# Performance work log

Hardware: AMD Instinct MI355X
Metric: run time of the kernel (lower is better)

The kernel has to match this reference:

```python
import jax, jax.numpy as jnp
import numpy as np

B, D_TCF, T, GAF_DIM, DK, HIDDEN, N_CLASSES = 128, 512, 1024, 256, 32, 64, 4
EPS = 1e-5

def _glorot(key, shape):
    fan_out, fan_in = shape
    lim = float(np.sqrt(6.0 / (fan_in + fan_out)))
    return jax.random.uniform(key, shape, jnp.float32, -lim, lim)

def setup_inputs() -> dict:
    key = jax.random.key(0)
    ks = jax.random.split(key, 8)
    return {
        "tcf_feat": jax.random.normal(ks[0], (B, D_TCF, T), jnp.float32),
        "gaf_emb": jax.random.normal(ks[1], (B, GAF_DIM), jnp.float32),
        "Wq": _glorot(ks[2], (DK, D_TCF)),        # q_proj.weight [out,in]
        "Wkv": _glorot(ks[3], (DK, GAF_DIM)),     # kv_proj.weight
        "Wout": _glorot(ks[4], (D_TCF, DK)),      # out_proj.weight
        "ln1_g": jnp.ones((D_TCF,), jnp.float32),
        "ln1_b": jnp.zeros((D_TCF,), jnp.float32),
        "W1": _glorot(ks[5], (HIDDEN, D_TCF)),
        "b1": jnp.zeros((HIDDEN,), jnp.float32),
        "ln2_g": jnp.ones((HIDDEN,), jnp.float32),
        "ln2_b": jnp.zeros((HIDDEN,), jnp.float32),
        "W2": _glorot(ks[6], (N_CLASSES, HIDDEN)),
        "b2": jnp.zeros((N_CLASSES,), jnp.float32),
    }

def _layernorm(x, g, b):
    mu = jnp.mean(x, axis=-1, keepdims=True)
    var = jnp.mean(jnp.square(x - mu), axis=-1, keepdims=True)
    return (x - mu) * jax.lax.rsqrt(var + EPS) * g + b

def reference(tcf_feat, gaf_emb, Wq, Wkv, Wout, ln1_g, ln1_b, W1, b1, ln2_g, ln2_b, W2, b2):
    scale = DK ** (-0.5)
    x = jnp.swapaxes(tcf_feat, 1, 2)                      # [B,T,d_tcf]
    Q = jnp.einsum('btd,kd->btk', x, Wq)                  # [B,T,dk]
    KV = gaf_emb @ Wkv.T                                  # [B,dk] (single key/value)
    scores = jnp.einsum('btk,bk->bt', Q, KV) * scale      # [B,T]
    w = jax.nn.softmax(scores, axis=1)                    # softmax over T (dim=1)
    attn_out = w[:, :, None] * KV[:, None, :]             # [B,T,dk]
    y = _layernorm(x + jnp.einsum('btk,dk->btd', attn_out, Wout), ln1_g, ln1_b)
    pooled = jnp.mean(y, axis=1)                          # [B,d_tcf]
    h = jax.nn.elu(_layernorm(pooled @ W1.T + b1, ln2_g, ln2_b))
    return h @ W2.T + b2                                  # [B,n_classes]
```

## Files before the change

kernel.cpp:

```cpp
#include <hip/hip_runtime.h>

#define BN 128
#define DTCF 512
#define TT 1024
#define GAF 256
#define DKK 32
#define HID 64
#define NCLS 4
#define LNEPS 1e-5f

__global__ __launch_bounds__(256) void k_prep(
    const float* __restrict__ gaf, const float* __restrict__ Wq,
    const float* __restrict__ Wkv, const float* __restrict__ Wout,
    float* __restrict__ u, float* __restrict__ qv,
    float* __restrict__ muu, float* __restrict__ varu)
{
    int b = blockIdx.x, tid = threadIdx.x;
    __shared__ float gaf_s[GAF];
    __shared__ float kv_s[DKK];
    __shared__ float red[16];

    gaf_s[tid & (GAF - 1)] = gaf[b * GAF + (tid & (GAF - 1))];
    __syncthreads();

    if (tid < DKK) {
        float acc = 0.f;
        for (int g = 0; g < GAF; ++g) acc += gaf_s[g] * Wkv[tid * GAF + g];
        kv_s[tid] = acc;
    }
    __syncthreads();

    float su = 0.f, suu = 0.f;
    for (int d = tid; d < DTCF; d += 256) {
        float uu = 0.f, qq = 0.f;
        #pragma unroll
        for (int k = 0; k < DKK; ++k) {
            float kv = kv_s[k];
            uu += kv * Wout[d * DKK + k];
            qq += kv * Wq[k * DTCF + d];
        }
        u[b * DTCF + d] = uu;
        qv[b * DTCF + d] = qq;
        su += uu; suu += uu * uu;
    }
    int lane = tid & 63, wv = tid >> 6;
    for (int off = 32; off > 0; off >>= 1) {
        su  += __shfl_down(su, off);
        suu += __shfl_down(suu, off);
    }
    if (lane == 0) { red[wv] = su; red[8 + wv] = suu; }
    __syncthreads();
    if (tid == 0) {
        float s  = red[0] + red[1] + red[2] + red[3];
        float ss = red[8] + red[9] + red[10] + red[11];
        float m = s * (1.f / DTCF);
        muu[b]  = m;
        varu[b] = ss * (1.f / DTCF) - m * m;
    }
}

__global__ __launch_bounds__(256) void k_passA(
    const float* __restrict__ tcf, const float* __restrict__ u,
    const float* __restrict__ qv, const float* __restrict__ muu,
    float* __restrict__ mx_o, float* __restrict__ varx_o,
    float* __restrict__ cov_o, float* __restrict__ score_o)
{
    int b = blockIdx.x, tc = blockIdx.y, tid = threadIdx.x;
    int t = tc * 256 + tid;
    __shared__ float u_s[DTCF], qv_s[DTCF];
    for (int i = tid; i < DTCF; i += 256) {
        u_s[i]  = u[b * DTCF + i];
        qv_s[i] = qv[b * DTCF + i];
    }
    __syncthreads();

    const float* base = tcf + (size_t)b * DTCF * TT + t;
    float sx = 0.f, sxx = 0.f, sxu = 0.f, sxq = 0.f;
    #pragma unroll 8
    for (int d = 0; d < DTCF; ++d) {
        float v = base[(size_t)d * TT];
        sx  += v;
        sxx += v * v;
        sxu += v * u_s[d];
        sxq += v * qv_s[d];
    }
    float mx = sx * (1.f / DTCF);
    size_t o = (size_t)b * TT + t;
    mx_o[o]    = mx;
    varx_o[o]  = sxx * (1.f / DTCF) - mx * mx;
    cov_o[o]   = sxu * (1.f / DTCF) - mx * muu[b];
    score_o[o] = sxq * 0.17677669529663687f;
}

__global__ __launch_bounds__(256) void k_soft(
    const float* __restrict__ score, const float* __restrict__ varx,
    const float* __restrict__ cov, const float* __restrict__ mx,
    const float* __restrict__ varu,
    float* __restrict__ r_o, float* __restrict__ S2, float* __restrict__ S3)
{
    int b = blockIdx.x, tid = threadIdx.x;
    int lane = tid & 63, wv = tid >> 6;
    __shared__ float red[16];
    const float* sc = score + (size_t)b * TT;

    float s0 = sc[tid], s1 = sc[tid + 256], s2v = sc[tid + 512], s3v = sc[tid + 768];
    float m = fmaxf(fmaxf(s0, s1), fmaxf(s2v, s3v));
    for (int off = 32; off > 0; off >>= 1) m = fmaxf(m, __shfl_xor(m, off));
    if (lane == 0) red[wv] = m;
    __syncthreads();
    m = fmaxf(fmaxf(red[0], red[1]), fmaxf(red[2], red[3]));

    float e0 = __expf(s0 - m), e1 = __expf(s1 - m);
    float e2 = __expf(s2v - m), e3 = __expf(s3v - m);
    float sum = e0 + e1 + e2 + e3;
    for (int off = 32; off > 0; off >>= 1) sum += __shfl_xor(sum, off);
    __syncthreads();
    if (lane == 0) red[4 + wv] = sum;
    __syncthreads();
    sum = red[4] + red[5] + red[6] + red[7];
    float inv = 1.f / sum;
    float vu = varu[b];

    float e[4] = {e0, e1, e2, e3};
    float s2a = 0.f, s3a = 0.f;
    #pragma unroll
    for (int i = 0; i < 4; ++i) {
        size_t o = (size_t)b * TT + tid + i * 256;
        float w = e[i] * inv;
        float vr = varx[o] + 2.f * w * cov[o] + w * w * vu;
        float rr = rsqrtf(vr + LNEPS);
        r_o[o] = rr;
        s2a += rr * w;
        s3a += rr * mx[o];
    }
    for (int off = 32; off > 0; off >>= 1) {
        s2a += __shfl_xor(s2a, off);
        s3a += __shfl_xor(s3a, off);
    }
    __syncthreads();
    if (lane == 0) { red[wv] = s2a; red[8 + wv] = s3a; }
    __syncthreads();
    if (tid == 0) {
        S2[b] = (red[0] + red[1] + red[2] + red[3]) * (1.f / TT);
        S3[b] = (red[8] + red[9] + red[10] + red[11]) * (1.f / TT);
    }
}

__global__ __launch_bounds__(256) void k_passB(
    const float* __restrict__ tcf, const float* __restrict__ r,
    const float* __restrict__ u, const float* __restrict__ muu,
    const float* __restrict__ S2, const float* __restrict__ S3,
    const float* __restrict__ g1, const float* __restrict__ be1,
    float* __restrict__ pooled)
{
    int b = blockIdx.x, dblk = blockIdx.y;
    int tid = threadIdx.x, wv = tid >> 6, lane = tid & 63;
    int d = dblk * 4 + wv;

    const float* row = tcf + ((size_t)b * DTCF + d) * TT + lane * 16;
    const float* rb  = r + (size_t)b * TT + lane * 16;

    float4 x0 = *(const float4*)(row);
    float4 x1 = *(const float4*)(row + 4);
    float4 x2 = *(const float4*)(row + 8);
    float4 x3 = *(const float4*)(row + 12);
    float4 r0 = *(const float4*)(rb);
    float4 r1 = *(const float4*)(rb + 4);
    float4 r2 = *(const float4*)(rb + 8);
    float4 r3 = *(const float4*)(rb + 12);

    float acc = 0.f;
    acc += r0.x * x0.x + r0.y * x0.y + r0.z * x0.z + r0.w * x0.w;
    acc += r1.x * x1.x + r1.y * x1.y + r1.z * x1.z + r1.w * x1.w;
    acc += r2.x * x2.x + r2.y * x2.y + r2.z * x2.z + r2.w * x2.w;
    acc += r3.x * x3.x + r3.y * x3.y + r3.z * x3.z + r3.w * x3.w;

    for (int off = 32; off > 0; off >>= 1) acc += __shfl_down(acc, off);

    if (lane == 0) {
        float pd = acc * (1.f / TT) - S3[b] + (u[b * DTCF + d] - muu[b]) * S2[b];
        pooled[b * DTCF + d] = g1[d] * pd + be1[d];
    }
}

__global__ __launch_bounds__(64) void k_head(
    const float* __restrict__ pooled, const float* __restrict__ W1,
    const float* __restrict__ b1, const float* __restrict__ g2,
    const float* __restrict__ be2, const float* __restrict__ W2,
    const float* __restrict__ b2o, float* __restrict__ out)
{
    int b = blockIdx.x, j = threadIdx.x;
    __shared__ float p_s[DTCF];
    for (int i = j; i < DTCF; i += 64) p_s[i] = pooled[b * DTCF + i];
    __syncthreads();

    float h = 0.f;
    for (int dd = 0; dd < DTCF; ++dd) h += p_s[dd] * W1[j * DTCF + dd];
    h += b1[j];

    float mu = h;
    for (int off = 32; off > 0; off >>= 1) mu += __shfl_xor(mu, off);
    mu *= (1.f / HID);
    float df = h - mu;
    float vr = df * df;
    for (int off = 32; off > 0; off >>= 1) vr += __shfl_xor(vr, off);
    vr *= (1.f / HID);
    float hn = df * rsqrtf(vr + LNEPS) * g2[j] + be2[j];
    float he = hn > 0.f ? hn : expm1f(hn);

    #pragma unroll
    for (int c = 0; c < NCLS; ++c) {
        float v = he * W2[c * HID + j];
        for (int off = 32; off > 0; off >>= 1) v += __shfl_xor(v, off);
        if (j == 0) out[b * NCLS + c] = v + b2o[c];
    }
}

extern "C" void kernel_launch(void* const* d_in, const int* in_sizes, int n_in,
                              void* d_out, int out_size, void* d_ws, size_t ws_size,
                              hipStream_t stream)
{
    const float* tcf  = (const float*)d_in[0];
    const float* gaf  = (const float*)d_in[1];
    const float* Wq   = (const float*)d_in[2];
    const float* Wkv  = (const float*)d_in[3];
    const float* Wout = (const float*)d_in[4];
    const float* ln1g = (const float*)d_in[5];
    const float* ln1b = (const float*)d_in[6];
    const float* W1   = (const float*)d_in[7];
    const float* b1   = (const float*)d_in[8];
    const float* ln2g = (const float*)d_in[9];
    const float* ln2b = (const float*)d_in[10];
    const float* W2   = (const float*)d_in[11];
    const float* b2   = (const float*)d_in[12];

    float* ws     = (float*)d_ws;
    float* u      = ws;
    float* qv     = u + BN * DTCF;
    float* muu    = qv + BN * DTCF;
    float* varu   = muu + BN;
    float* mx     = varu + BN;
    float* varx   = mx + BN * TT;
    float* cov    = varx + BN * TT;
    float* score  = cov + BN * TT;
    float* r      = score + BN * TT;
    float* S2     = r + BN * TT;
    float* S3     = S2 + BN;
    float* pooled = S3 + BN;

    k_prep<<<BN, 256, 0, stream>>>(gaf, Wq, Wkv, Wout, u, qv, muu, varu);
    k_passA<<<dim3(BN, TT / 256), 256, 0, stream>>>(tcf, u, qv, muu, mx, varx, cov, score);
    k_soft<<<BN, 256, 0, stream>>>(score, varx, cov, mx, varu, r, S2, S3);
    k_passB<<<dim3(BN, DTCF / 4), 256, 0, stream>>>(tcf, r, u, muu, S2, S3, ln1g, ln1b, pooled);
    k_head<<<BN, 64, 0, stream>>>(pooled, W1, b1, ln2g, ln2b, W2, b2, (float*)d_out);
}
```

Baseline: 446.0 us.

## Split passA over D chunks with float4 loads and fold stats into softmax

passA now splits the 512-wide feature dimension into 8 chunks per batch and uses float4 loads along T. It writes partial sums (sx, sxx, sxu, sxq) that k_soft reduces before deriving mean, variance, covariance and scores. The change also spreads the KV projection in k_prep over all threads, transposes W1 in extra k_prep blocks, widens k_head to 256 threads using the transposed W1, and switches passB to coalesced strided float4 loads. The goal is more parallelism and wider memory accesses in the bandwidth-bound passes, at the cost of an extra partial-sum buffer round trip.

```diff
diff --git a/kernel.cpp b/kernel.cpp
--- a/kernel.cpp
+++ b/kernel.cpp
@@ -8,25 +8,51 @@
 #define HID 64
 #define NCLS 4
 #define LNEPS 1e-5f
+#define DC 8
+#define DCL (DTCF/DC)
 
 __global__ __launch_bounds__(256) void k_prep(
     const float* __restrict__ gaf, const float* __restrict__ Wq,
     const float* __restrict__ Wkv, const float* __restrict__ Wout,
+    const float* __restrict__ W1,
     float* __restrict__ u, float* __restrict__ qv,
-    float* __restrict__ muu, float* __restrict__ varu)
+    float* __restrict__ muu, float* __restrict__ varu,
+    float* __restrict__ W1t)
 {
     int b = blockIdx.x, tid = threadIdx.x;
+
+    if (b >= BN) {
+        int e0 = (b - BN) * 4096 + tid * 16;
+        int j  = e0 >> 9;
+        int dd = e0 & 511;
+        #pragma unroll
+        for (int i = 0; i < 16; ++i)
+            W1t[(dd + i) * HID + j] = W1[j * DTCF + dd + i];
+        return;
+    }
+
     __shared__ float gaf_s[GAF];
+    __shared__ float kvp[DKK][9];
     __shared__ float kv_s[DKK];
     __shared__ float red[16];
 
     gaf_s[tid & (GAF - 1)] = gaf[b * GAF + (tid & (GAF - 1))];
     __syncthreads();
 
+    {
+        int k = tid >> 3, p8 = tid & 7;
+        float acc = 0.f;
+        #pragma unroll
+        for (int g = p8 * 32; g < p8 * 32 + 32; ++g)
+            acc += gaf_s[g] * Wkv[k * GAF + g];
+        kvp[k][p8] = acc;
+    }
+    __syncthreads();
     if (tid < DKK) {
-        float acc = 0.f;
-        for (int g = 0; g < GAF; ++g) acc += gaf_s[g] * Wkv[tid * GAF + g];
-        kv_s[tid] = acc;
+        float a = 0.f;
+        #pragma unroll
+        for (int p = 0; p < 8; ++p) a += kvp[tid][p];
+        kv_s[tid] = a;
     }
     __syncthreads();
 
@@ -61,88 +87,107 @@
 
 __global__ __launch_bounds__(256) void k_passA(
     const float* __restrict__ tcf, const float* __restrict__ u,
-    const float* __restrict__ qv, const float* __restrict__ muu,
-    float* __restrict__ mx_o, float* __restrict__ varx_o,
-    float* __restrict__ cov_o, float* __restrict__ score_o)
-{
-    int b = blockIdx.x, tc = blockIdx.y, tid = threadIdx.x;
-    int t = tc * 256 + tid;
-    __shared__ float u_s[DTCF], qv_s[DTCF];
-    for (int i = tid; i < DTCF; i += 256) {
-        u_s[i]  = u[b * DTCF + i];
-        qv_s[i] = qv[b * DTCF + i];
-    }
-    __syncthreads();
-
-    const float* base = tcf + (size_t)b * DTCF * TT + t;
-    float sx = 0.f, sxx = 0.f, sxu = 0.f, sxq = 0.f;
-    #pragma unroll 8
-    for (int d = 0; d < DTCF; ++d) {
-        float v = base[(size_t)d * TT];
-        sx  += v;
-        sxx += v * v;
-        sxu += v * u_s[d];
-        sxq += v * qv_s[d];
-    }
-    float mx = sx * (1.f / DTCF);
-    size_t o = (size_t)b * TT + t;
-    mx_o[o]    = mx;
-    varx_o[o]  = sxx * (1.f / DTCF) - mx * mx;
-    cov_o[o]   = sxu * (1.f / DTCF) - mx * muu[b];
-    score_o[o] = sxq * 0.17677669529663687f;
+    const float* __restrict__ qv, float* __restrict__ part)
+{
+    int b = blockIdx.x, dc = blockIdx.y, tid = threadIdx.x;
+    __shared__ float u_s[DCL], qv_s[DCL];
+    if (tid < DCL) u_s[tid] = u[b * DTCF + dc * DCL + tid];
+    else if (tid < 2 * DCL) qv_s[tid - DCL] = qv[b * DTCF + dc * DCL + (tid - DCL)];
+    __syncthreads();
+
+    int t0 = tid * 4;
+    const float* base = tcf + ((size_t)b * DTCF + dc * DCL) * TT + t0;
+    float4 sx = {0,0,0,0}, sxx = {0,0,0,0}, sxu = {0,0,0,0}, sxq = {0,0,0,0};
+    #pragma unroll 4
+    for (int d = 0; d < DCL; ++d) {
+        float4 v = *(const float4*)(base + (size_t)d * TT);
+        float uu = u_s[d], qq = qv_s[d];
+        sx.x += v.x; sx.y += v.y; sx.z += v.z; sx.w += v.w;
+        sxx.x += v.x*v.x; sxx.y += v.y*v.y; sxx.z += v.z*v.z; sxx.w += v.w*v.w;
+        sxu.x += v.x*uu; sxu.y += v.y*uu; sxu.z += v.z*uu; sxu.w += v.w*uu;
+        sxq.x += v.x*qq; sxq.y += v.y*qq; sxq.z += v.z*qq; sxq.w += v.w*qq;
+    }
+    float* p = part + (((size_t)b * DC + dc) * 4) * TT + t0;
+    *(float4*)(p)          = sx;
+    *(float4*)(p + TT)     = sxx;
+    *(float4*)(p + 2 * TT) = sxu;
+    *(float4*)(p + 3 * TT) = sxq;
 }
 
 __global__ __launch_bounds__(256) void k_soft(
-    const float* __restrict__ score, const float* __restrict__ varx,
-    const float* __restrict__ cov, const float* __restrict__ mx,
+    const float* __restrict__ part, const float* __restrict__ muu,
     const float* __restrict__ varu,
     float* __restrict__ r_o, float* __restrict__ S2, float* __restrict__ S3)
 {
     int b = blockIdx.x, tid = threadIdx.x;
     int lane = tid & 63, wv = tid >> 6;
     __shared__ float red[16];
-    const float* sc = score + (size_t)b * TT;
-
-    float s0 = sc[tid], s1 = sc[tid + 256], s2v = sc[tid + 512], s3v = sc[tid + 768];
-    float m = fmaxf(fmaxf(s0, s1), fmaxf(s2v, s3v));
+    int t0 = tid * 4;
+
+    float4 sx = {0,0,0,0}, sxx = {0,0,0,0}, sxu = {0,0,0,0}, sxq = {0,0,0,0};
+    #pragma unroll
+    for (int dc = 0; dc < DC; ++dc) {
+        const float* p = part + (((size_t)b * DC + dc) * 4) * TT + t0;
+        float4 a = *(const float4*)(p);
+        float4 bq = *(const float4*)(p + TT);
+        float4 c = *(const float4*)(p + 2 * TT);
+        float4 dq = *(const float4*)(p + 3 * TT);
+        sx.x += a.x; sx.y += a.y; sx.z += a.z; sx.w += a.w;
+        sxx.x += bq.x; sxx.y += bq.y; sxx.z += bq.z; sxx.w += bq.w;
+        sxu.x += c.x; sxu.y += c.y; sxu.z += c.z; sxu.w += c.w;
+        sxq.x += dq.x; sxq.y += dq.y; sxq.z += dq.z; sxq.w += dq.w;
+    }
+    float mu = muu[b], vu = varu[b];
+    const float inv_d = 1.f / DTCF, scale = 0.17677669529663687f;
+    float mx[4], vx[4], cv[4], sc[4];
+    float sxa[4] = {sx.x, sx.y, sx.z, sx.w};
+    float sxxa[4] = {sxx.x, sxx.y, sxx.z, sxx.w};
+    float sxua[4] = {sxu.x, sxu.y, sxu.z, sxu.w};
+    float sxqa[4] = {sxq.x, sxq.y, sxq.z, sxq.w};
+    #pragma unroll
+    for (int i = 0; i < 4; ++i) {
+        mx[i] = sxa[i] * inv_d;
+        vx[i] = sxxa[i] * inv_d - mx[i] * mx[i];
+        cv[i] = sxua[i] * inv_d - mx[i] * mu;
+        sc[i] = sxqa[i] * scale;
+    }
+
+    float m = fmaxf(fmaxf(sc[0], sc[1]), fmaxf(sc[2], sc[3]));
     for (int off = 32; off > 0; off >>= 1) m = fmaxf(m, __shfl_xor(m, off));
     if (lane == 0) red[wv] = m;
     __syncthreads();
     m = fmaxf(fmaxf(red[0], red[1]), fmaxf(red[2], red[3]));
 
-    float e0 = __expf(s0 - m), e1 = __expf(s1 - m);
-    float e2 = __expf(s2v - m), e3 = __expf(s3v - m);
-    float sum = e0 + e1 + e2 + e3;
+    float e[4], sum = 0.f;
+    #pragma unroll
+    for (int i = 0; i < 4; ++i) { e[i] = __expf(sc[i] - m); sum += e[i]; }
     for (int off = 32; off > 0; off >>= 1) sum += __shfl_xor(sum, off);
-    __syncthreads();
     if (lane == 0) red[4 + wv] = sum;
     __syncthreads();
     sum = red[4] + red[5] + red[6] + red[7];
     float inv = 1.f / sum;
-    float vu = varu[b];
-
-    float e[4] = {e0, e1, e2, e3};
-    float s2a = 0.f, s3a = 0.f;
+
+    float rr4[4], s2a = 0.f, s3a = 0.f;
     #pragma unroll
     for (int i = 0; i < 4; ++i) {
-        size_t o = (size_t)b * TT + tid + i * 256;
         float w = e[i] * inv;
-        float vr = varx[o] + 2.f * w * cov[o] + w * w * vu;
+        float vr = vx[i] + 2.f * w * cv[i] + w * w * vu;
         float rr = rsqrtf(vr + LNEPS);
-        r_o[o] = rr;
+        rr4[i] = rr;
         s2a += rr * w;
-        s3a += rr * mx[o];
-    }
+        s3a += rr * mx[i];
+    }
+    *(float4*)(r_o + (size_t)b * TT + t0) = make_float4(rr4[0], rr4[1], rr4[2], rr4[3]);
+
     for (int off = 32; off > 0; off >>= 1) {
         s2a += __shfl_xor(s2a, off);
         s3a += __shfl_xor(s3a, off);
     }
-    __syncthreads();
-    if (lane == 0) { red[wv] = s2a; red[8 + wv] = s3a; }
+    if (lane == 0) { red[8 + wv] = s2a; red[12 + wv] = s3a; }
     __syncthreads();
     if (tid == 0) {
-        S2[b] = (red[0] + red[1] + red[2] + red[3]) * (1.f / TT);
-        S3[b] = (red[8] + red[9] + red[10] + red[11]) * (1.f / TT);
+        S2[b] = (red[8] + red[9] + red[10] + red[11]) * (1.f / TT);
+        S3[b] = (red[12] + red[13] + red[14] + red[15]) * (1.f / TT);
     }
 }
 
@@ -157,24 +202,16 @@
     int tid = threadIdx.x, wv = tid >> 6, lane = tid & 63;
     int d = dblk * 4 + wv;
 
-    const float* row = tcf + ((size_t)b * DTCF + d) * TT + lane * 16;
-    const float* rb  = r + (size_t)b * TT + lane * 16;
-
-    float4 x0 = *(const float4*)(row);
-    float4 x1 = *(const float4*)(row + 4);
-    float4 x2 = *(const float4*)(row + 8);
-    float4 x3 = *(const float4*)(row + 12);
-    float4 r0 = *(const float4*)(rb);
-    float4 r1 = *(const float4*)(rb + 4);
-    float4 r2 = *(const float4*)(rb + 8);
-    float4 r3 = *(const float4*)(rb + 12);
+    const float* row = tcf + ((size_t)b * DTCF + d) * TT;
+    const float* rb  = r + (size_t)b * TT;
 
     float acc = 0.f;
-    acc += r0.x * x0.x + r0.y * x0.y + r0.z * x0.z + r0.w * x0.w;
-    acc += r1.x * x1.x + r1.y * x1.y + r1.z * x1.z + r1.w * x1.w;
-    acc += r2.x * x2.x + r2.y * x2.y + r2.z * x2.z + r2.w * x2.w;
-    acc += r3.x * x3.x + r3.y * x3.y + r3.z * x3.z + r3.w * x3.w;
-
+    #pragma unroll
+    for (int i = 0; i < 4; ++i) {
+        float4 x = *(const float4*)(row + i * 256 + lane * 4);
+        float4 rv = *(const float4*)(rb + i * 256 + lane * 4);
+        acc += rv.x * x.x + rv.y * x.y + rv.z * x.z + rv.w * x.w;
+    }
     for (int off = 32; off > 0; off >>= 1) acc += __shfl_down(acc, off);
 
     if (lane == 0) {
@@ -183,36 +220,46 @@
     }
 }
 
-__global__ __launch_bounds__(64) void k_head(
-    const float* __restrict__ pooled, const float* __restrict__ W1,
+__global__ __launch_bounds__(256) void k_head(
+    const float* __restrict__ pooled, const float* __restrict__ W1t,
     const float* __restrict__ b1, const float* __restrict__ g2,
     const float* __restrict__ be2, const float* __restrict__ W2,
     const float* __restrict__ b2o, float* __restrict__ out)
 {
-    int b = blockIdx.x, j = threadIdx.x;
+    int b = blockIdx.x, tid = threadIdx.x;
+    int j = tid & 63, wv = tid >> 6;
     __shared__ float p_s[DTCF];
-    for (int i = j; i < DTCF; i += 64) p_s[i] = pooled[b * DTCF + i];
-    __syncthreads();
-
-    float h = 0.f;
-    for (int dd = 0; dd < DTCF; ++dd) h += p_s[dd] * W1[j * DTCF + dd];
-    h += b1[j];
-
-    float mu = h;
-    for (int off = 32; off > 0; off >>= 1) mu += __shfl_xor(mu, off);
-    mu *= (1.f / HID);
-    float df = h - mu;
-    float vr = df * df;
-    for (int off = 32; off > 0; off >>= 1) vr += __shfl_xor(vr, off);
-    vr *= (1.f / HID);
-    float hn = df * rsqrtf(vr + LNEPS) * g2[j] + be2[j];
-    float he = hn > 0.f ? hn : expm1f(hn);
-
-    #pragma unroll
-    for (int c = 0; c < NCLS; ++c) {
-        float v = he * W2[c * HID + j];
-        for (int off = 32; off > 0; off >>= 1) v += __shfl_xor(v, off);
-        if (j == 0) out[b * NCLS + c] = v + b2o[c];
+    __shared__ float hred[4][HID];
+    for (int i = tid; i < DTCF; i += 256) p_s[i] = pooled[b * DTCF + i];
+    __syncthreads();
+
+    float hp = 0.f;
+    #pragma unroll 8
+    for (int i = 0; i < 128; ++i) {
+        int dd = wv * 128 + i;
+        hp += p_s[dd] * W1t[dd * HID + j];
+    }
+    hred[wv][j] = hp;
+    __syncthreads();
+
+    if (wv == 0) {
+        float h = hred[0][j] + hred[1][j] + hred[2][j] + hred[3][j] + b1[j];
+        float mu = h;
+        for (int off = 32; off > 0; off >>= 1) mu += __shfl_xor(mu, off);
+        mu *= (1.f / HID);
+        float df = h - mu;
+        float vr = df * df;
+        for (int off = 32; off > 0; off >>= 1) vr += __shfl_xor(vr, off);
+        vr *= (1.f / HID);
+        float hn = df * rsqrtf(vr + LNEPS) * g2[j] + be2[j];
+        float he = hn > 0.f ? hn : expm1f(hn);
+
+        #pragma unroll
+        for (int c = 0; c < NCLS; ++c) {
+            float v = he * W2[c * HID + j];
+            for (int off = 32; off > 0; off >>= 1) v += __shfl_xor(v, off);
+            if (j == 0) out[b * NCLS + c] = v + b2o[c];
+        }
     }
 }
 
@@ -239,18 +286,16 @@
     float* qv     = u + BN * DTCF;
     float* muu    = qv + BN * DTCF;
     float* varu   = muu + BN;
-    float* mx     = varu + BN;
-    float* varx   = mx + BN * TT;
-    float* cov    = varx + BN * TT;
-    float* score  = cov + BN * TT;
-    float* r      = score + BN * TT;
+    float* r      = varu + BN;
     float* S2     = r + BN * TT;
     float* S3     = S2 + BN;
     float* pooled = S3 + BN;
-
-    k_prep<<<BN, 256, 0, stream>>>(gaf, Wq, Wkv, Wout, u, qv, muu, varu);
-    k_passA<<<dim3(BN, TT / 256), 256, 0, stream>>>(tcf, u, qv, muu, mx, varx, cov, score);
-    k_soft<<<BN, 256, 0, stream>>>(score, varx, cov, mx, varu, r, S2, S3);
+    float* W1t    = pooled + BN * DTCF;
+    float* part   = W1t + DTCF * HID;
+
+    k_prep<<<BN + 8, 256, 0, stream>>>(gaf, Wq, Wkv, Wout, W1, u, qv, muu, varu, W1t);
+    k_passA<<<dim3(BN, DC), 256, 0, stream>>>(tcf, u, qv, part);
+    k_soft<<<BN, 256, 0, stream>>>(part, muu, varu, r, S2, S3);
     k_passB<<<dim3(BN, DTCF / 4), 256, 0, stream>>>(tcf, r, u, muu, S2, S3, ln1g, ln1b, pooled);
-    k_head<<<BN, 64, 0, stream>>>(pooled, W1, b1, ln2g, ln2b, W2, b2, (float*)d_out);
-}
+    k_head<<<BN, 256, 0, stream>>>(pooled, W1t, b1, ln2g, ln2b, W2, b2, (float*)d_out);
+}
```

After: 444.3 us. About the same (-0.4%).
